# Optimization experiments

Hardware: AMD Instinct MI355X
Metric: run time of the kernel (lower is better)

Reference implementation:

```python
import jax, jax.numpy as jnp
import numpy as np

B, C, H, W = 16, 256, 128, 128  # ration = 1 -> C' = C


def setup_inputs() -> dict:
    key = jax.random.key(0)
    ks = jax.random.split(key, 7)
    s = 1.0 / np.sqrt(C)
    return {
        "x": jax.random.normal(ks[0], (B, C, H, W), dtype=jnp.float32),
        "Wq": jax.random.normal(ks[1], (C, C), dtype=jnp.float32) * s,
        "Wk": jax.random.normal(ks[2], (C, C), dtype=jnp.float32) * s,
        "Wv": jax.random.normal(ks[3], (C, C), dtype=jnp.float32) * s,
        "gamma": jax.random.normal(ks[4], (1,), dtype=jnp.float32) * 0.1,
        "Wup": jax.random.normal(ks[5], (C, C), dtype=jnp.float32) * s,
        "b_up": jax.random.normal(ks[6], (C,), dtype=jnp.float32) * 0.01,
    }


def reference(x, Wq, Wk, Wv, gamma, Wup, b_up):
    b, c, h, w = x.shape
    # 1x1 conv (no bias) == channel-mixing einsum, followed by ReLU
    proj = lambda Wm: jax.nn.relu(jnp.einsum('oc,bchw->bohw', Wm, x))
    # torch .view(B, H, -1) is a raw row-major reinterpretation of [B,C,H,W]
    q = proj(Wq).reshape(b, h, -1)                      # [B, H, C*W]
    k = proj(Wk).reshape(b, h, -1).transpose(0, 2, 1)   # [B, C*W, H]
    v = proj(Wv).reshape(b, h, -1).transpose(0, 2, 1)   # [B, C*W, H]
    # non-standard softmax over dim=1 (rows of the HxH score matrix)
    attn = jax.nn.softmax(jnp.matmul(q, k), axis=1)     # [B, H, H]
    out1 = jnp.matmul(v, attn)                          # [B, C*W, H]
    out_h = out1.reshape(b, c, h, w) * gamma            # raw reshape, gamma scale
    # layer_up: 1x1 conv with bias
    out_h = jnp.einsum('oc,bchw->bohw', Wup, out_h) + b_up[None, :, None, None]
    return (out_h, q, k, v, gamma, attn)
```

## Files before the change

kernel.cpp:

```cpp
#include <hip/hip_runtime.h>
#include <stdint.h>


typedef _Float16 f16;
typedef __attribute__((ext_vector_type(8))) _Float16 f16x8;
typedef __attribute__((ext_vector_type(4))) float f32x4;

#define DEV static __device__ __forceinline__

constexpr int  HW   = 16384;
constexpr long PB   = 4194304;
constexpr long HALF = 2097152;

constexpr long WH_OFF  = 0;
constexpr long WL_OFF  = 393216;
constexpr long WU_OFF  = 786432;
constexpr long H16_OFF = 1048576;
constexpr long WS_NEED = H16_OFF + 134217728L;

DEV unsigned pk2(float a, float b) {
  auto h = __builtin_amdgcn_cvt_pkrtz(a, b);
  return __builtin_bit_cast(unsigned, h);
}
DEV void split_pk2(float a, float b, unsigned& hu, unsigned& lu) {
  auto h = __builtin_amdgcn_cvt_pkrtz(a, b);
  auto l = __builtin_amdgcn_cvt_pkrtz(a - (float)h[0], b - (float)h[1]);
  hu = __builtin_bit_cast(unsigned, h);
  lu = __builtin_bit_cast(unsigned, l);
}
DEV f32x4 mfma16(f16x8 a, f16x8 b, f32x4 c) {
  return __builtin_amdgcn_mfma_f32_16x16x32_f16(a, b, c, 0, 0, 0);
}
DEV f16x8 ld64(const char* base, int row, int g) {
  return *(const f16x8*)(base + row * 64 + 16 * (g ^ ((row >> 1) & 3)));
}
DEV int swz64off(int row, int g) { return row * 64 + 16 * (g ^ ((row >> 1) & 3)); }

DEV void gload16(const void* g, void* l) {
  __builtin_amdgcn_global_load_lds(
      (const __attribute__((address_space(1))) uint32_t*)(g),
      (__attribute__((address_space(3))) uint32_t*)(l), 16, 0, 0);
}

DEV int swz(int row, int kbyte) {
  return (kbyte & ~63) | ((kbyte & 63) ^ (((row >> 3) & 3) << 4));
}
DEV f16x8 ldfrag(const f16* arr, int strideB, int row, int kbyte) {
  return *(const f16x8*)((const char*)arr + row * strideB + swz(row, kbyte));
}

__global__ __launch_bounds__(256) void prep_w(
    const float* __restrict__ Wq, const float* __restrict__ Wk,
    const float* __restrict__ Wv, const float* __restrict__ Wu,
    const float* __restrict__ gin, char* __restrict__ ws) {
  const int kc = blockIdx.x, m = blockIdx.y, o = threadIdx.x;
  const float* src = (m == 0) ? Wq : (m == 1) ? Wk : (m == 2) ? Wv : Wu;
  const float sc = (m == 3) ? gin[0] : 1.0f;
  float v[32];
#pragma unroll
  for (int j = 0; j < 32; ++j) v[j] = src[o * 256 + kc * 32 + j] * sc;
  char* dh = (m < 3) ? (ws + WH_OFF + ((long)(m * 8 + kc) * 256 + o) * 64)
                     : (ws + WU_OFF + ((long)kc * 256 + o) * 64);
  char* dl = ws + WL_OFF + ((long)(m * 8 + kc) * 256 + o) * 64;
  const int sw = (o >> 1) & 3;
#pragma unroll
  for (int gq = 0; gq < 4; ++gq) {
    unsigned h[4], l[4];
#pragma unroll
    for (int p = 0; p < 4; ++p)
      split_pk2(v[8 * gq + 2 * p], v[8 * gq + 2 * p + 1], h[p], l[p]);
    const int off = 16 * (gq ^ sw);
    *(uint4*)(dh + off) = make_uint4(h[0], h[1], h[2], h[3]);
    if (m < 3) *(uint4*)(dl + off) = make_uint4(l[0], l[1], l[2], l[3]);
  }
}

__global__ __launch_bounds__(256, 2) void qkv_fused2(
    const float* __restrict__ x,
    const char* __restrict__ wqh, const char* __restrict__ wql,
    const char* __restrict__ wkh, const char* __restrict__ wkl,
    const char* __restrict__ wvh,
    float* __restrict__ qseg, float* __restrict__ kseg,
    float* __restrict__ vseg) {
  __shared__ char Xh[32768];
  __shared__ char Xl[32768];
  const int t = threadIdx.x, lane = t & 63, w = t >> 6;
  const int l15 = lane & 15, g = lane >> 4;
  const int b = blockIdx.y, hw0 = blockIdx.x * 64;
  const float* xb = x + (long)b * PB + hw0;

  {
    const int hw = t & 63, cq = t >> 6;
    const int sw = (hw >> 1) & 3;
#pragma unroll
    for (int j8 = 0; j8 < 8; ++j8) {
      const int c0 = cq * 64 + j8 * 8;
      float v[8];
#pragma unroll
      for (int i = 0; i < 8; ++i) v[i] = xb[(long)(c0 + i) * HW + hw];
      unsigned h[4], l[4];
#pragma unroll
      for (int p = 0; p < 4; ++p)
        split_pk2(v[2 * p], v[2 * p + 1], h[p], l[p]);
      const int kc = c0 >> 5, gi = (c0 >> 3) & 3;
      const int off = kc * 4096 + hw * 64 + 16 * (gi ^ sw);
      *(uint4*)(Xh + off) = make_uint4(h[0], h[1], h[2], h[3]);
      *(uint4*)(Xl + off) = make_uint4(l[0], l[1], l[2], l[3]);
    }
  }
  __syncthreads();

  {
    f32x4 acc[4][4] = {};
    for (int kc = 0; kc < 8; ++kc) {
      const char* XH = Xh + kc * 4096;
      const char* XL = Xl + kc * 4096;
      const char* WH = wqh + (long)kc * 16384;
      const char* WL = wql + (long)kc * 16384;
      f16x8 bh[4], bl[4];
#pragma unroll
      for (int nf = 0; nf < 4; ++nf) {
        bh[nf] = ld64(XH, 16 * nf + l15, g);
        bl[nf] = ld64(XL, 16 * nf + l15, g);
      }
#pragma unroll
      for (int mf = 0; mf < 4; ++mf) {
        const int orow = w * 64 + 16 * mf + l15;
        f16x8 ah = ld64(WH, orow, g);
        f16x8 al = ld64(WL, orow, g);
#pragma unroll
        for (int nf = 0; nf < 4; ++nf) {
          acc[mf][nf] = mfma16(ah, bh[nf], acc[mf][nf]);
          acc[mf][nf] = mfma16(ah, bl[nf], acc[mf][nf]);
          acc[mf][nf] = mfma16(al, bh[nf], acc[mf][nf]);
        }
      }
    }
    float* ob = qseg + (long)b * PB;
#pragma unroll
    for (int mf = 0; mf < 4; ++mf)
#pragma unroll
      for (int nf = 0; nf < 4; ++nf)
#pragma unroll
        for (int r = 0; r < 4; ++r) {
          float v = acc[mf][nf][r];
          v = v > 0.f ? v : 0.f;
          const int o = w * 64 + 16 * mf + 4 * g + r;
          const int hw = hw0 + 16 * nf + l15;
          ob[(long)o * HW + hw] = v;
        }
  }

  {
    f32x4 acc[4][4] = {};
    for (int kc = 0; kc < 8; ++kc) {
      const char* XH = Xh + kc * 4096;
      const char* XL = Xl + kc * 4096;
      const char* WH = wkh + (long)kc * 16384;
      const char* WL = wkl + (long)kc * 16384;
      f16x8 bh[4], bl[4];
#pragma unroll
      for (int nf = 0; nf < 4; ++nf) {
        const int orow = w * 64 + 16 * nf + l15;
        bh[nf] = ld64(WH, orow, g);
        bl[nf] = ld64(WL, orow, g);
      }
#pragma unroll
      for (int mf = 0; mf < 4; ++mf) {
        f16x8 ah = ld64(XH, 16 * mf + l15, g);
        f16x8 al = ld64(XL, 16 * mf + l15, g);
#pragma unroll
        for (int nf = 0; nf < 4; ++nf) {
          acc[mf][nf] = mfma16(ah, bh[nf], acc[mf][nf]);
          acc[mf][nf] = mfma16(ah, bl[nf], acc[mf][nf]);
          acc[mf][nf] = mfma16(al, bh[nf], acc[mf][nf]);
        }
      }
    }
    float* ob = kseg + (long)b * PB;
#pragma unroll
    for (int mf = 0; mf < 4; ++mf)
#pragma unroll
      for (int nf = 0; nf < 4; ++nf)
#pragma unroll
        for (int r = 0; r < 4; ++r) {
          float v = acc[mf][nf][r];
          v = v > 0.f ? v : 0.f;
          const int hw = hw0 + 16 * mf + 4 * g + r;
          const int o = w * 64 + 16 * nf + l15;
          ob[((o & 1) ? HALF : 0) + (long)hw * 128 + (o >> 1)] = v;
        }
  }

  {
    f32x4 acc[4][4] = {};
    for (int kc = 0; kc < 8; ++kc) {
      const char* XH = Xh + kc * 4096;
      const char* WH = wvh + (long)kc * 16384;
      f16x8 bh[4];
#pragma unroll
      for (int nf = 0; nf < 4; ++nf)
        bh[nf] = ld64(WH, w * 64 + 16 * nf + l15, g);
#pragma unroll
      for (int mf = 0; mf < 4; ++mf) {
        f16x8 ah = ld64(XH, 16 * mf + l15, g);
#pragma unroll
        for (int nf = 0; nf < 4; ++nf)
          acc[mf][nf] = mfma16(ah, bh[nf], acc[mf][nf]);
      }
    }
    float* ob = vseg + (long)b * PB;
#pragma unroll
    for (int mf = 0; mf < 4; ++mf)
#pragma unroll
      for (int nf = 0; nf < 4; ++nf)
#pragma unroll
        for (int r = 0; r < 4; ++r) {
          float v = acc[mf][nf][r];
          v = v > 0.f ? v : 0.f;
          const int hw = hw0 + 16 * mf + 4 * g + r;
          const int o = w * 64 + 16 * nf + l15;
          ob[((o & 1) ? HALF : 0) + (long)hw * 128 + (o >> 1)] = v;
        }
  }
}

__global__ __launch_bounds__(256) void spart_kernel(
    const float* __restrict__ qseg, const float* __restrict__ kseg,
    float* __restrict__ part) {
  constexpr int SB = 80;
  __shared__ f16 Ah[128 * 40], Al[128 * 40], Bh[128 * 40], Bl[128 * 40];
  const int t = threadIdx.x, lane = t & 63, w = t >> 6;
  const int l15 = lane & 15, g = lane >> 4;
  const int ch = blockIdx.x, b = blockIdx.y;
  const float* qb = qseg + (long)b * PB + ch * 1024;
  const float* kb = kseg + (long)b * PB + (long)ch * 1024 * 128;

  f32x4 acc[4][4] = {};

  for (int kc = 0; kc < 1024; kc += 32) {
#pragma unroll
    for (int it = 0; it < 4; ++it) {
      int f4 = t + 256 * it;
      int i = f4 >> 3, c4 = f4 & 7;
      float4 v = *(const float4*)(qb + (long)i * 32768 + kc + 4 * c4);
      unsigned h01, l01, h23, l23;
      split_pk2(v.x, v.y, h01, l01);
      split_pk2(v.z, v.w, h23, l23);
      int kbo = swz(i, 8 * c4);
      *(uint2*)((char*)Ah + i * SB + kbo) = make_uint2(h01, h23);
      *(uint2*)((char*)Al + i * SB + kbo) = make_uint2(l01, l23);
    }
    {
      int c = t & 127, rh = t >> 7;
      float vs[16];
#pragma unroll
      for (int r = 0; r < 16; ++r)
        vs[r] = kb[(long)(kc + 16 * rh + r) * 128 + c];
#pragma unroll
      for (int u = 0; u < 4; ++u) {
        unsigned h0, l0, h1, l1;
        split_pk2(vs[4 * u], vs[4 * u + 1], h0, l0);
        split_pk2(vs[4 * u + 2], vs[4 * u + 3], h1, l1);
        int kbo = swz(c, 32 * rh + 8 * u);
        *(uint2*)((char*)Bh + c * SB + kbo) = make_uint2(h0, h1);
        *(uint2*)((char*)Bl + c * SB + kbo) = make_uint2(l0, l1);
      }
    }
    __syncthreads();

    f16x8 afh[4], afl[4], bfh[4], bfl[4];
#pragma unroll
    for (int f = 0; f < 4; ++f) {
      int ar = (w & 1) * 64 + 16 * f + l15;
      int br = (w >> 1) * 64 + 16 * f + l15;
      afh[f] = ldfrag(Ah, SB, ar, 16 * g);
      afl[f] = ldfrag(Al, SB, ar, 16 * g);
      bfh[f] = ldfrag(Bh, SB, br, 16 * g);
      bfl[f] = ldfrag(Bl, SB, br, 16 * g);
    }
#pragma unroll
    for (int mf = 0; mf < 4; ++mf)
#pragma unroll
      for (int nf = 0; nf < 4; ++nf) {
        acc[mf][nf] = mfma16(afh[mf], bfh[nf], acc[mf][nf]);
        acc[mf][nf] = mfma16(afh[mf], bfl[nf], acc[mf][nf]);
        acc[mf][nf] = mfma16(afl[mf], bfh[nf], acc[mf][nf]);
      }
    __syncthreads();
  }

  float* pp = part + (long)(b * 32 + ch) * 16384;
#pragma unroll
  for (int mf = 0; mf < 4; ++mf)
#pragma unroll
    for (int nf = 0; nf < 4; ++nf)
#pragma unroll
      for (int r = 0; r < 4; ++r) {
        int i = (w & 1) * 64 + 16 * mf + 4 * g + r;
        int i2 = (w >> 1) * 64 + 16 * nf + l15;
        pp[i * 128 + i2] = acc[mf][nf][r];
      }
}

__global__ __launch_bounds__(128) void reduce_s(
    const float* __restrict__ part, float* __restrict__ att,
    float* __restrict__ gout, const float* __restrict__ gin) {
  const int i = blockIdx.x, b = blockIdx.y, t = threadIdx.x;
  if (b == 0 && i == 0 && t == 0) gout[0] = gin[0];
  const float* pp = part + (long)b * 524288 + i * 128 + t;
  float s = 0.f;
#pragma unroll
  for (int c = 0; c < 32; ++c) s += pp[(long)c * 16384];
  att[((long)b * 128 + i) * 128 + t] = s;
}

__global__ __launch_bounds__(256) void softmax2(float* __restrict__ att) {
  __shared__ float red[16][17];
  const int b = blockIdx.y, c0 = blockIdx.x * 16;
  const int t = threadIdx.x, col = t & 15, ig = t >> 4;
  float* ab = att + (long)b * 16384 + c0 + col;
  float s[8];
  float m = -3.0e38f;
#pragma unroll
  for (int j = 0; j < 8; ++j) {
    s[j] = ab[(ig * 8 + j) * 128];
    m = fmaxf(m, s[j]);
  }
  red[ig][col] = m;
  __syncthreads();
  float mx = red[0][col];
#pragma unroll
  for (int k = 1; k < 16; ++k) mx = fmaxf(mx, red[k][col]);
  float sum = 0.f;
#pragma unroll
  for (int j = 0; j < 8; ++j) {
    s[j] = expf(s[j] - mx);
    sum += s[j];
  }
  __syncthreads();
  red[ig][col] = sum;
  __syncthreads();
  float tot = 0.f;
#pragma unroll
  for (int k = 0; k < 16; ++k) tot += red[k][col];
  float inv = 1.f / tot;
#pragma unroll
  for (int j = 0; j < 8; ++j) ab[(ig * 8 + j) * 128] = s[j] * inv;
}

template <int F16OUT>
__global__ __launch_bounds__(256) void out1_kernel(
    const float* __restrict__ vseg, const float* __restrict__ att,
    void* __restrict__ outp) {
  constexpr int SB = 272;
  __shared__ f16 Va[64 * 136], Ba[128 * 136];
  const int t = threadIdx.x, lane = t & 63, w = t >> 6;
  const int l15 = lane & 15, g = lane >> 4;
  const int b = blockIdx.y;
  const long j0 = (long)blockIdx.x * 64;
  const float* vb = vseg + (long)b * PB + j0 * 128;
  const float* ab = att + (long)b * 16384;

#pragma unroll
  for (int it = 0; it < 8; ++it) {
    int f4 = t + 256 * it;
    int j = f4 >> 5, c4 = f4 & 31;
    float4 v = *(const float4*)(vb + (long)j * 128 + 4 * c4);
    int kb = swz(j, 8 * c4);
    *(uint2*)((char*)Va + j * SB + kb) = make_uint2(pk2(v.x, v.y), pk2(v.z, v.w));
  }
  {
    int c = t & 127, rh = t >> 7;
#pragma unroll
    for (int uu = 0; uu < 16; ++uu) {
      int i0 = 64 * rh + 4 * uu;
      float v0 = ab[(i0 + 0) * 128 + c];
      float v1 = ab[(i0 + 1) * 128 + c];
      float v2 = ab[(i0 + 2) * 128 + c];
      float v3 = ab[(i0 + 3) * 128 + c];
      int kb = swz(c, 2 * i0);
      *(uint2*)((char*)Ba + c * SB + kb) = make_uint2(pk2(v0, v1), pk2(v2, v3));
    }
  }
  __syncthreads();

  f32x4 acc[2][4] = {};
#pragma unroll
  for (int kf = 0; kf < 4; ++kf) {
    f16x8 af[2], bf[4];
#pragma unroll
    for (int mf = 0; mf < 2; ++mf)
      af[mf] = ldfrag(Va, SB, (w & 1) * 32 + 16 * mf + l15, 64 * kf + 16 * g);
#pragma unroll
    for (int nf = 0; nf < 4; ++nf)
      bf[nf] = ldfrag(Ba, SB, (w >> 1) * 64 + 16 * nf + l15, 64 * kf + 16 * g);
#pragma unroll
    for (int mf = 0; mf < 2; ++mf)
#pragma unroll
      for (int nf = 0; nf < 4; ++nf)
        acc[mf][nf] = mfma16(af[mf], bf[nf], acc[mf][nf]);
  }

#pragma unroll
  for (int mf = 0; mf < 2; ++mf)
#pragma unroll
    for (int nf = 0; nf < 4; ++nf)
#pragma unroll
      for (int r = 0; r < 4; ++r) {
        long j = j0 + (w & 1) * 32 + 16 * mf + 4 * g + r;
        int i2 = (w >> 1) * 64 + 16 * nf + l15;
        if constexpr (F16OUT) {
          f16* ob = (f16*)outp + (long)b * PB;
          ob[j * 128 + i2] = (f16)acc[mf][nf][r];
        } else {
          float* ob = (float*)outp + (long)b * PB;
          ob[j * 128 + i2] = acc[mf][nf][r];
        }
      }
}

__global__ __launch_bounds__(256) void final3(
    float* __restrict__ outseg, const f16* __restrict__ h16,
    const char* __restrict__ wu, const float* __restrict__ bup) {
  __shared__ char lds[16384 + 4096];
  const int t = threadIdx.x, lane = t & 63, w = t >> 6;
  const int l15 = lane & 15, g = lane >> 4;
  const int b = blockIdx.y, hw0 = blockIdx.x * 64;
  const unsigned short* Hb = (const unsigned short*)(h16 + (long)b * PB);
  float* Ob = outseg + (long)b * PB;
  char* ldsA = lds;
  char* ldsB = lds + 16384;
  const int n = t & 63, rq = t >> 6;

  f32x4 acc[4][4] = {};
  for (int kc = 0; kc < 8; ++kc) {
#pragma unroll
    for (int i = 0; i < 4; ++i)
      gload16(wu + (long)kc * 16384 + w * 4096 + i * 1024 + lane * 16,
              ldsA + w * 4096 + i * 1024);
    {
      unsigned short us[8];
#pragma unroll
      for (int j = 0; j < 8; ++j)
        us[j] = Hb[(long)(kc * 32 + rq * 8 + j) * HW + hw0 + n];
      unsigned u[4];
#pragma unroll
      for (int p = 0; p < 4; ++p)
        u[p] = (unsigned)us[2 * p] | ((unsigned)us[2 * p + 1] << 16);
      *(uint4*)(ldsB + swz64off(n, rq)) = make_uint4(u[0], u[1], u[2], u[3]);
    }
    __syncthreads();
    f16x8 bf[4];
#pragma unroll
    for (int nf = 0; nf < 4; ++nf) bf[nf] = ld64(ldsB, 16 * nf + l15, g);
#pragma unroll
    for (int mf = 0; mf < 4; ++mf) {
      f16x8 af = ld64(ldsA, 64 * w + 16 * mf + l15, g);
#pragma unroll
      for (int nf = 0; nf < 4; ++nf)
        acc[mf][nf] = mfma16(af, bf[nf], acc[mf][nf]);
    }
    __syncthreads();
  }

#pragma unroll
  for (int mf = 0; mf < 4; ++mf)
#pragma unroll
    for (int nf = 0; nf < 4; ++nf)
#pragma unroll
      for (int r = 0; r < 4; ++r) {
        int o = 64 * w + 16 * mf + 4 * g + r;
        int hw = hw0 + 16 * nf + l15;
        Ob[(long)o * HW + hw] = acc[mf][nf][r] + bup[o];
      }
}

__global__ __launch_bounds__(128) void softmax_kernel(
    const float* __restrict__ part, float* __restrict__ att,
    float* __restrict__ gout, const float* __restrict__ gin) {
  const int b = blockIdx.x, t = threadIdx.x;
  if (b == 0 && t == 0) gout[0] = gin[0];
  const float* pp = part + (long)b * 32 * 16384;
  float* ab = att + (long)b * 16384;
  float mx = -3.0e38f;
  for (int i = 0; i < 128; ++i) {
    float s = 0.f;
#pragma unroll
    for (int c = 0; c < 32; ++c) s += pp[(long)c * 16384 + i * 128 + t];
    ab[i * 128 + t] = s;
    mx = fmaxf(mx, s);
  }
  float sum = 0.f;
  for (int i = 0; i < 128; ++i) {
    float e = expf(ab[i * 128 + t] - mx);
    sum += e;
    ab[i * 128 + t] = e;
  }
  float inv = 1.f / sum;
  for (int i = 0; i < 128; ++i) ab[i * 128 + t] *= inv;
}

template <int MODE>
__global__ __launch_bounds__(256) void proj_kernel(
    const float* __restrict__ x, const float* __restrict__ Wm,
    float* __restrict__ out) {
  constexpr int SB = 80;
  __shared__ f16 Wh[256 * 40];
  __shared__ f16 Wl[256 * 40];
  __shared__ f16 Xh[64 * 40];
  __shared__ f16 Xl[64 * 40];

  const int t = threadIdx.x;
  const int lane = t & 63;
  const int w = t >> 6;
  const int l15 = lane & 15;
  const int g = lane >> 4;
  const int b = blockIdx.y;
  const int hw0 = blockIdx.x * 64;
  const float* xb = x + (long)b * PB;

  f32x4 acc[4][4] = {};

  for (int kc = 0; kc < 256; kc += 32) {
#pragma unroll
    for (int it = 0; it < 8; ++it) {
      int f4 = t + 256 * it;
      int o = f4 >> 3, c4 = f4 & 7;
      float4 v = *(const float4*)(Wm + o * 256 + kc + 4 * c4);
      unsigned h01, l01, h23, l23;
      split_pk2(v.x, v.y, h01, l01);
      split_pk2(v.z, v.w, h23, l23);
      int kb = swz(o, 8 * c4);
      *(uint2*)((char*)Wh + o * SB + kb) = make_uint2(h01, h23);
      *(uint2*)((char*)Wl + o * SB + kb) = make_uint2(l01, l23);
    }
    {
      int c = t & 63, rq = t >> 6;
      float vs[8];
#pragma unroll
      for (int r = 0; r < 8; ++r)
        vs[r] = xb[(long)(kc + 8 * rq + r) * HW + hw0 + c];
#pragma unroll
      for (int u = 0; u < 2; ++u) {
        unsigned h0, l0, h1, l1;
        split_pk2(vs[4 * u], vs[4 * u + 1], h0, l0);
        split_pk2(vs[4 * u + 2], vs[4 * u + 3], h1, l1);
        int kb = swz(c, 16 * rq + 8 * u);
        *(uint2*)((char*)Xh + c * SB + kb) = make_uint2(h0, h1);
        *(uint2*)((char*)Xl + c * SB + kb) = make_uint2(l0, l1);
      }
    }
    __syncthreads();

    f16x8 wfh[4], wfl[4], xfh[4], xfl[4];
#pragma unroll
    for (int f = 0; f < 4; ++f) {
      int wr = 64 * w + 16 * f + l15;
      int xr = 16 * f + l15;
      wfh[f] = ldfrag(Wh, SB, wr, 16 * g);
      wfl[f] = ldfrag(Wl, SB, wr, 16 * g);
      xfh[f] = ldfrag(Xh, SB, xr, 16 * g);
      xfl[f] = ldfrag(Xl, SB, xr, 16 * g);
    }
#pragma unroll
    for (int mf = 0; mf < 4; ++mf)
#pragma unroll
      for (int nf = 0; nf < 4; ++nf) {
        if constexpr (MODE == 0) {
          acc[mf][nf] = mfma16(wfh[mf], xfh[nf], acc[mf][nf]);
          acc[mf][nf] = mfma16(wfh[mf], xfl[nf], acc[mf][nf]);
          acc[mf][nf] = mfma16(wfl[mf], xfh[nf], acc[mf][nf]);
        } else {
          acc[mf][nf] = mfma16(xfh[mf], wfh[nf], acc[mf][nf]);
          acc[mf][nf] = mfma16(xfh[mf], wfl[nf], acc[mf][nf]);
          acc[mf][nf] = mfma16(xfl[mf], wfh[nf], acc[mf][nf]);
        }
      }
    __syncthreads();
  }

  float* ob = out + (long)b * PB;
#pragma unroll
  for (int mf = 0; mf < 4; ++mf)
#pragma unroll
    for (int nf = 0; nf < 4; ++nf)
#pragma unroll
      for (int r = 0; r < 4; ++r) {
        float v = acc[mf][nf][r];
        v = v > 0.f ? v : 0.f;
        if constexpr (MODE == 0) {
          int o = 64 * w + 16 * mf + 4 * g + r;
          int hw = hw0 + 16 * nf + l15;
          ob[(long)o * HW + hw] = v;
        } else {
          int hw = hw0 + 16 * mf + 4 * g + r;
          int o = 64 * w + 16 * nf + l15;
          ob[((o & 1) ? HALF : 0) + (long)hw * 128 + (o >> 1)] = v;
        }
      }
}

__global__ __launch_bounds__(256) void final_kernel(
    float* __restrict__ outseg, const float* __restrict__ Wup,
    const float* __restrict__ bup, const float* __restrict__ gin) {
  constexpr int SB = 144;
  __shared__ f16 Ah[256 * 72], Bh[64 * 72];
  const int t = threadIdx.x, lane = t & 63, w = t >> 6;
  const int l15 = lane & 15, g = lane >> 4;
  const int b = blockIdx.y;
  const int hw0 = blockIdx.x * 64;
  const float gamma = gin[0];
  float* Hb = outseg + (long)b * PB;

  f32x4 acc[4][4] = {};

  for (int kc = 0; kc < 256; kc += 64) {
#pragma unroll
    for (int it = 0; it < 16; ++it) {
      int f4 = t + 256 * it;
      int o = f4 >> 4, c4 = f4 & 15;
      float4 v = *(const float4*)(Wup + o * 256 + kc + 4 * c4);
      int kb = swz(o, 8 * c4);
      *(uint2*)((char*)Ah + o * SB + kb) =
          make_uint2(pk2(v.x * gamma, v.y * gamma), pk2(v.z * gamma, v.w * gamma));
    }
    {
      int n = t & 63, rq = t >> 6;
#pragma unroll
      for (int uu = 0; uu < 4; ++uu) {
        int r0 = 16 * rq + 4 * uu;
        float v0 = Hb[(long)(kc + r0 + 0) * HW + hw0 + n];
        float v1 = Hb[(long)(kc + r0 + 1) * HW + hw0 + n];
        float v2 = Hb[(long)(kc + r0 + 2) * HW + hw0 + n];
        float v3 = Hb[(long)(kc + r0 + 3) * HW + hw0 + n];
        int kb = swz(n, 2 * r0);
        *(uint2*)((char*)Bh + n * SB + kb) = make_uint2(pk2(v0, v1), pk2(v2, v3));
      }
    }
    __syncthreads();

    f16x8 af[4][2], bf[4][2];
#pragma unroll
    for (int f = 0; f < 4; ++f)
#pragma unroll
      for (int kf = 0; kf < 2; ++kf) {
        af[f][kf] = ldfrag(Ah, SB, 64 * w + 16 * f + l15, 64 * kf + 16 * g);
        bf[f][kf] = ldfrag(Bh, SB, 16 * f + l15, 64 * kf + 16 * g);
      }
#pragma unroll
    for (int mf = 0; mf < 4; ++mf)
#pragma unroll
      for (int nf = 0; nf < 4; ++nf) {
        acc[mf][nf] = mfma16(af[mf][0], bf[nf][0], acc[mf][nf]);
        acc[mf][nf] = mfma16(af[mf][1], bf[nf][1], acc[mf][nf]);
      }
    __syncthreads();
  }

#pragma unroll
  for (int mf = 0; mf < 4; ++mf)
#pragma unroll
    for (int nf = 0; nf < 4; ++nf)
#pragma unroll
      for (int r = 0; r < 4; ++r) {
        int o = 64 * w + 16 * mf + 4 * g + r;
        int hw = hw0 + 16 * nf + l15;
        Hb[(long)o * HW + hw] = acc[mf][nf][r] + bup[o];
      }
}

extern "C" void kernel_launch(void* const* d_in, const int* in_sizes, int n_in,
                              void* d_out, int out_size, void* d_ws, size_t ws_size,
                              hipStream_t stream) {
  (void)in_sizes; (void)n_in; (void)out_size;

  const float* x  = (const float*)d_in[0];
  const float* Wq = (const float*)d_in[1];
  const float* Wk = (const float*)d_in[2];
  const float* Wv = (const float*)d_in[3];
  const float* gm = (const float*)d_in[4];
  const float* Wu = (const float*)d_in[5];
  const float* bu = (const float*)d_in[6];

  float* out  = (float*)d_out;
  float* oseg = out;
  float* qseg = out + 67108864L;
  float* kseg = out + 134217728L;
  float* vseg = out + 201326592L;
  float* gseg = out + 268435456L;
  float* aseg = out + 268435457L;

  dim3 blk(256);
  if (ws_size >= (size_t)WS_NEED && d_ws != nullptr) {
    char* ws = (char*)d_ws;
    prep_w<<<dim3(8, 4), blk, 0, stream>>>(Wq, Wk, Wv, Wu, gm, ws);
    qkv_fused2<<<dim3(256, 16), blk, 0, stream>>>(
        x, ws + WH_OFF, ws + WL_OFF, ws + WH_OFF + 131072, ws + WL_OFF + 131072,
        ws + WH_OFF + 262144, qseg, kseg, vseg);
    spart_kernel<<<dim3(32, 16), blk, 0, stream>>>(qseg, kseg, oseg);
    reduce_s<<<dim3(128, 16), dim3(128), 0, stream>>>(oseg, aseg, gseg, gm);
    softmax2<<<dim3(8, 16), blk, 0, stream>>>(aseg);
    out1_kernel<1><<<dim3(512, 16), blk, 0, stream>>>(vseg, aseg, ws + H16_OFF);
    final3<<<dim3(256, 16), blk, 0, stream>>>(
        oseg, (const f16*)(ws + H16_OFF), ws + WU_OFF, bu);
  } else {
    proj_kernel<0><<<dim3(256, 16), blk, 0, stream>>>(x, Wq, qseg);
    proj_kernel<1><<<dim3(256, 16), blk, 0, stream>>>(x, Wk, kseg);
    proj_kernel<1><<<dim3(256, 16), blk, 0, stream>>>(x, Wv, vseg);
    spart_kernel<<<dim3(32, 16), blk, 0, stream>>>(qseg, kseg, oseg);
    softmax_kernel<<<dim3(16), dim3(128), 0, stream>>>(oseg, aseg, gseg, gm);
    out1_kernel<0><<<dim3(512, 16), blk, 0, stream>>>(vseg, aseg, oseg);
    final_kernel<<<dim3(256, 16), blk, 0, stream>>>(oseg, Wu, bu, gm);
  }
}
```

Measured before the change: 707.9 us.

## Fuse attention-V matmul with up-projection and coalesce K/V stores via LDS

Replaces the separate out1 (fp16 intermediate in workspace) and final up-projection kernels with one kernel per (batch, h) row. It computes V·attn for 64-channel chunks into LDS and immediately multiplies by the fp16 Wup, so the 128 MB fp16 intermediate never goes to global memory. Separately, the K and V projection epilogues now stage ReLU results through swizzled LDS and write coalesced float4 rows instead of scattered scalar stores. The costs are extra barriers, lower occupancy from large LDS use, and a serial chunk loop inside the fused kernel.

Result: faster. 672.6 us (-5.0%).

```diff
diff --git a/kernel.cpp b/kernel.cpp
--- a/kernel.cpp
+++ b/kernel.cpp
@@ -15,8 +15,7 @@
 constexpr long WH_OFF  = 0;
 constexpr long WL_OFF  = 393216;
 constexpr long WU_OFF  = 786432;
-constexpr long H16_OFF = 1048576;
-constexpr long WS_NEED = H16_OFF + 134217728L;
+constexpr long WS_NEED = 1048576;
 
 DEV unsigned pk2(float a, float b) {
   auto h = __builtin_amdgcn_cvt_pkrtz(a, b);
@@ -34,7 +33,6 @@
 DEV f16x8 ld64(const char* base, int row, int g) {
   return *(const f16x8*)(base + row * 64 + 16 * (g ^ ((row >> 1) & 3)));
 }
-DEV int swz64off(int row, int g) { return row * 64 + 16 * (g ^ ((row >> 1) & 3)); }
 
 DEV void gload16(const void* g, void* l) {
   __builtin_amdgcn_global_load_lds(
@@ -75,15 +73,17 @@
   }
 }
 
-__global__ __launch_bounds__(256, 2) void qkv_fused2(
+__global__ __launch_bounds__(256, 2) void qkv_fused3(
     const float* __restrict__ x,
     const char* __restrict__ wqh, const char* __restrict__ wql,
     const char* __restrict__ wkh, const char* __restrict__ wkl,
     const char* __restrict__ wvh,
     float* __restrict__ qseg, float* __restrict__ kseg,
     float* __restrict__ vseg) {
-  __shared__ char Xh[32768];
-  __shared__ char Xl[32768];
+  __shared__ char lds[65536];
+  char* Xh = lds;
+  char* Xl = lds + 32768;
+  float* R = (float*)(lds + 32768);
   const int t = threadIdx.x, lane = t & 63, w = t >> 6;
   const int l15 = lane & 15, g = lane >> 4;
   const int b = blockIdx.y, hw0 = blockIdx.x * 64;
@@ -109,6 +109,37 @@
     }
   }
   __syncthreads();
+
+  auto repack_store = [&](f32x4 (&ac)[4][4], float* ob) {
+#pragma unroll
+    for (int half = 0; half < 2; ++half) {
+#pragma unroll
+      for (int mf2 = 0; mf2 < 2; ++mf2) {
+        const int mf = 2 * half + mf2;
+#pragma unroll
+        for (int nf = 0; nf < 4; ++nf)
+#pragma unroll
+          for (int r = 0; r < 4; ++r) {
+            const int hwloc = 16 * mf2 + 4 * g + r;
+            const int o = w * 64 + 16 * nf + l15;
+            const int col = (o >> 1) ^ (((hwloc >> 2) & 3) << 3);
+            float v = ac[mf][nf][r];
+            R[(o & 1) * 4096 + hwloc * 128 + col] = v > 0.f ? v : 0.f;
+          }
+      }
+      __syncthreads();
+#pragma unroll
+      for (int it = 0; it < 8; ++it) {
+        const int f = t + 256 * it;
+        const int parity = f >> 10, hwloc = (f >> 5) & 31, q4 = f & 31;
+        const int col = (4 * q4) ^ (((hwloc >> 2) & 3) << 3);
+        const float4 v4 = *(const float4*)(R + parity * 4096 + hwloc * 128 + col);
+        *(float4*)(ob + (long)parity * HALF +
+                   (long)(hw0 + 32 * half + hwloc) * 128 + 4 * q4) = v4;
+      }
+      __syncthreads();
+    }
+  };
 
   {
     f32x4 acc[4][4] = {};
@@ -177,19 +208,8 @@
         }
       }
     }
-    float* ob = kseg + (long)b * PB;
-#pragma unroll
-    for (int mf = 0; mf < 4; ++mf)
-#pragma unroll
-      for (int nf = 0; nf < 4; ++nf)
-#pragma unroll
-        for (int r = 0; r < 4; ++r) {
-          float v = acc[mf][nf][r];
-          v = v > 0.f ? v : 0.f;
-          const int hw = hw0 + 16 * mf + 4 * g + r;
-          const int o = w * 64 + 16 * nf + l15;
-          ob[((o & 1) ? HALF : 0) + (long)hw * 128 + (o >> 1)] = v;
-        }
+    __syncthreads();
+    repack_store(acc, kseg + (long)b * PB);
   }
 
   {
@@ -209,19 +229,7 @@
           acc[mf][nf] = mfma16(ah, bh[nf], acc[mf][nf]);
       }
     }
-    float* ob = vseg + (long)b * PB;
-#pragma unroll
-    for (int mf = 0; mf < 4; ++mf)
-#pragma unroll
-      for (int nf = 0; nf < 4; ++nf)
-#pragma unroll
-        for (int r = 0; r < 4; ++r) {
-          float v = acc[mf][nf][r];
-          v = v > 0.f ? v : 0.f;
-          const int hw = hw0 + 16 * mf + 4 * g + r;
-          const int o = w * 64 + 16 * nf + l15;
-          ob[((o & 1) ? HALF : 0) + (long)hw * 128 + (o >> 1)] = v;
-        }
+    repack_store(acc, vseg + (long)b * PB);
   }
 }
 
@@ -349,130 +357,98 @@
   for (int j = 0; j < 8; ++j) ab[(ig * 8 + j) * 128] = s[j] * inv;
 }
 
-template <int F16OUT>
-__global__ __launch_bounds__(256) void out1_kernel(
+__global__ __launch_bounds__(256, 2) void pvf_fused(
     const float* __restrict__ vseg, const float* __restrict__ att,
-    void* __restrict__ outp) {
-  constexpr int SB = 272;
-  __shared__ f16 Va[64 * 136], Ba[128 * 136];
+    const char* __restrict__ wu, const float* __restrict__ bup,
+    float* __restrict__ oseg) {
+  __shared__ char attnT[128 * 272];
+  __shared__ char vA[64 * 272];
+  __shared__ char HT[128 * 144];
   const int t = threadIdx.x, lane = t & 63, w = t >> 6;
   const int l15 = lane & 15, g = lane >> 4;
-  const int b = blockIdx.y;
-  const long j0 = (long)blockIdx.x * 64;
-  const float* vb = vseg + (long)b * PB + j0 * 128;
+  const int b = blockIdx.y, h = blockIdx.x;
   const float* ab = att + (long)b * 16384;
-
-#pragma unroll
-  for (int it = 0; it < 8; ++it) {
-    int f4 = t + 256 * it;
-    int j = f4 >> 5, c4 = f4 & 31;
-    float4 v = *(const float4*)(vb + (long)j * 128 + 4 * c4);
-    int kb = swz(j, 8 * c4);
-    *(uint2*)((char*)Va + j * SB + kb) = make_uint2(pk2(v.x, v.y), pk2(v.z, v.w));
-  }
-  {
-    int c = t & 127, rh = t >> 7;
-#pragma unroll
-    for (int uu = 0; uu < 16; ++uu) {
-      int i0 = 64 * rh + 4 * uu;
-      float v0 = ab[(i0 + 0) * 128 + c];
-      float v1 = ab[(i0 + 1) * 128 + c];
-      float v2 = ab[(i0 + 2) * 128 + c];
-      float v3 = ab[(i0 + 3) * 128 + c];
-      int kb = swz(c, 2 * i0);
-      *(uint2*)((char*)Ba + c * SB + kb) = make_uint2(pk2(v0, v1), pk2(v2, v3));
-    }
-  }
-  __syncthreads();
-
-  f32x4 acc[2][4] = {};
-#pragma unroll
-  for (int kf = 0; kf < 4; ++kf) {
-    f16x8 af[2], bf[4];
-#pragma unroll
-    for (int mf = 0; mf < 2; ++mf)
-      af[mf] = ldfrag(Va, SB, (w & 1) * 32 + 16 * mf + l15, 64 * kf + 16 * g);
-#pragma unroll
-    for (int nf = 0; nf < 4; ++nf)
-      bf[nf] = ldfrag(Ba, SB, (w >> 1) * 64 + 16 * nf + l15, 64 * kf + 16 * g);
-#pragma unroll
-    for (int mf = 0; mf < 2; ++mf)
-#pragma unroll
-      for (int nf = 0; nf < 4; ++nf)
-        acc[mf][nf] = mfma16(af[mf], bf[nf], acc[mf][nf]);
-  }
-
-#pragma unroll
-  for (int mf = 0; mf < 2; ++mf)
-#pragma unroll
-    for (int nf = 0; nf < 4; ++nf)
+  const float* vb = vseg + (long)b * PB;
+  float* Ob = oseg + (long)b * PB;
+
+#pragma unroll
+  for (int it = 0; it < 4; ++it) {
+    const int f = t + 256 * it;
+    const int i4 = f >> 5, w4 = f & 31;
+    const float4 r0 = *(const float4*)(ab + (4 * i4 + 0) * 128 + 4 * w4);
+    const float4 r1 = *(const float4*)(ab + (4 * i4 + 1) * 128 + 4 * w4);
+    const float4 r2 = *(const float4*)(ab + (4 * i4 + 2) * 128 + 4 * w4);
+    const float4 r3 = *(const float4*)(ab + (4 * i4 + 3) * 128 + 4 * w4);
+    *(uint2*)(attnT + (4 * w4 + 0) * 272 + swz(4 * w4 + 0, 8 * i4)) =
+        make_uint2(pk2(r0.x, r1.x), pk2(r2.x, r3.x));
+    *(uint2*)(attnT + (4 * w4 + 1) * 272 + swz(4 * w4 + 1, 8 * i4)) =
+        make_uint2(pk2(r0.y, r1.y), pk2(r2.y, r3.y));
+    *(uint2*)(attnT + (4 * w4 + 2) * 272 + swz(4 * w4 + 2, 8 * i4)) =
+        make_uint2(pk2(r0.z, r1.z), pk2(r2.z, r3.z));
+    *(uint2*)(attnT + (4 * w4 + 3) * 272 + swz(4 * w4 + 3, 8 * i4)) =
+        make_uint2(pk2(r0.w, r1.w), pk2(r2.w, r3.w));
+  }
+
+  f32x4 acc2[4][8] = {};
+
+  for (int cc = 0; cc < 4; ++cc) {
+#pragma unroll
+    for (int it = 0; it < 8; ++it) {
+      const int f = t + 256 * it;
+      const int cp = f >> 5, q4 = f & 31;
+      const float4 v4 =
+          *(const float4*)(vb + ((long)(cc * 64 + cp) * 128 + h) * 128 + 4 * q4);
+      *(uint2*)(vA + cp * 272 + swz(cp, 8 * q4)) =
+          make_uint2(pk2(v4.x, v4.y), pk2(v4.z, v4.w));
+    }
+    __syncthreads();
+
+    f32x4 acc1[8] = {};
+#pragma unroll
+    for (int kf = 0; kf < 4; ++kf) {
+      const f16x8 a = ldfrag((const f16*)vA, 272, w * 16 + l15, 64 * kf + 16 * g);
+#pragma unroll
+      for (int nf = 0; nf < 8; ++nf) {
+        const f16x8 bf = ldfrag((const f16*)attnT, 272, 16 * nf + l15, 64 * kf + 16 * g);
+        acc1[nf] = mfma16(a, bf, acc1[nf]);
+      }
+    }
+#pragma unroll
+    for (int nf = 0; nf < 8; ++nf)
 #pragma unroll
       for (int r = 0; r < 4; ++r) {
-        long j = j0 + (w & 1) * 32 + 16 * mf + 4 * g + r;
-        int i2 = (w >> 1) * 64 + 16 * nf + l15;
-        if constexpr (F16OUT) {
-          f16* ob = (f16*)outp + (long)b * PB;
-          ob[j * 128 + i2] = (f16)acc[mf][nf][r];
-        } else {
-          float* ob = (float*)outp + (long)b * PB;
-          ob[j * 128 + i2] = acc[mf][nf][r];
-        }
-      }
-}
-
-__global__ __launch_bounds__(256) void final3(
-    float* __restrict__ outseg, const f16* __restrict__ h16,
-    const char* __restrict__ wu, const float* __restrict__ bup) {
-  __shared__ char lds[16384 + 4096];
-  const int t = threadIdx.x, lane = t & 63, w = t >> 6;
-  const int l15 = lane & 15, g = lane >> 4;
-  const int b = blockIdx.y, hw0 = blockIdx.x * 64;
-  const unsigned short* Hb = (const unsigned short*)(h16 + (long)b * PB);
-  float* Ob = outseg + (long)b * PB;
-  char* ldsA = lds;
-  char* ldsB = lds + 16384;
-  const int n = t & 63, rq = t >> 6;
-
-  f32x4 acc[4][4] = {};
-  for (int kc = 0; kc < 8; ++kc) {
-#pragma unroll
-    for (int i = 0; i < 4; ++i)
-      gload16(wu + (long)kc * 16384 + w * 4096 + i * 1024 + lane * 16,
-              ldsA + w * 4096 + i * 1024);
-    {
-      unsigned short us[8];
-#pragma unroll
-      for (int j = 0; j < 8; ++j)
-        us[j] = Hb[(long)(kc * 32 + rq * 8 + j) * HW + hw0 + n];
-      unsigned u[4];
-#pragma unroll
-      for (int p = 0; p < 4; ++p)
-        u[p] = (unsigned)us[2 * p] | ((unsigned)us[2 * p + 1] << 16);
-      *(uint4*)(ldsB + swz64off(n, rq)) = make_uint4(u[0], u[1], u[2], u[3]);
-    }
-    __syncthreads();
-    f16x8 bf[4];
-#pragma unroll
-    for (int nf = 0; nf < 4; ++nf) bf[nf] = ld64(ldsB, 16 * nf + l15, g);
-#pragma unroll
-    for (int mf = 0; mf < 4; ++mf) {
-      f16x8 af = ld64(ldsA, 64 * w + 16 * mf + l15, g);
-#pragma unroll
-      for (int nf = 0; nf < 4; ++nf)
-        acc[mf][nf] = mfma16(af, bf[nf], acc[mf][nf]);
-    }
-    __syncthreads();
+        const int wp = 16 * nf + l15;
+        const int cp = w * 16 + 4 * g + r;
+        *(f16*)(HT + wp * 144 + swz(wp, 2 * cp)) = (f16)acc1[nf][r];
+      }
+    __syncthreads();
+
+#pragma unroll
+    for (int kf2 = 0; kf2 < 2; ++kf2) {
+      const char* WU = wu + (long)(cc * 2 + kf2) * 16384;
+      f16x8 af[4];
+#pragma unroll
+      for (int mf = 0; mf < 4; ++mf)
+        af[mf] = ld64(WU, w * 64 + 16 * mf + l15, g);
+#pragma unroll
+      for (int nf = 0; nf < 8; ++nf) {
+        const f16x8 bf = ldfrag((const f16*)HT, 144, 16 * nf + l15, 64 * kf2 + 16 * g);
+#pragma unroll
+        for (int mf = 0; mf < 4; ++mf)
+          acc2[mf][nf] = mfma16(af[mf], bf, acc2[mf][nf]);
+      }
+    }
   }
 
 #pragma unroll
   for (int mf = 0; mf < 4; ++mf)
 #pragma unroll
-    for (int nf = 0; nf < 4; ++nf)
+    for (int nf = 0; nf < 8; ++nf)
 #pragma unroll
       for (int r = 0; r < 4; ++r) {
-        int o = 64 * w + 16 * mf + 4 * g + r;
-        int hw = hw0 + 16 * nf + l15;
-        Ob[(long)o * HW + hw] = acc[mf][nf][r] + bup[o];
+        const int o = w * 64 + 16 * mf + 4 * g + r;
+        const int wp = 16 * nf + l15;
+        Ob[(long)o * HW + h * 128 + wp] = acc2[mf][nf][r] + bup[o];
       }
 }
 
@@ -601,6 +577,71 @@
       }
 }
 
+__global__ __launch_bounds__(256) void out1_fb(
+    const float* __restrict__ vseg, const float* __restrict__ att,
+    float* __restrict__ outseg) {
+  constexpr int SB = 272;
+  __shared__ f16 Va[64 * 136], Ba[128 * 136];
+  const int t = threadIdx.x, lane = t & 63, w = t >> 6;
+  const int l15 = lane & 15, g = lane >> 4;
+  const int b = blockIdx.y;
+  const long j0 = (long)blockIdx.x * 64;
+  const float* vb = vseg + (long)b * PB + j0 * 128;
+  const float* ab = att + (long)b * 16384;
+
+#pragma unroll
+  for (int it = 0; it < 8; ++it) {
+    int f4 = t + 256 * it;
+    int j = f4 >> 5, c4 = f4 & 31;
+    float4 v = *(const float4*)(vb + (long)j * 128 + 4 * c4);
+    int kb = swz(j, 8 * c4);
+    *(uint2*)((char*)Va + j * SB + kb) = make_uint2(pk2(v.x, v.y), pk2(v.z, v.w));
+  }
+  {
+    int c = t & 127, rh = t >> 7;
+#pragma unroll
+    for (int uu = 0; uu < 16; ++uu) {
+      int i0 = 64 * rh + 4 * uu;
+      float v0 = ab[(i0 + 0) * 128 + c];
+      float v1 = ab[(i0 + 1) * 128 + c];
+      float v2 = ab[(i0 + 2) * 128 + c];
+      float v3 = ab[(i0 + 3) * 128 + c];
+      int kb = swz(c, 2 * i0);
+      *(uint2*)((char*)Ba + c * SB + kb) = make_uint2(pk2(v0, v1), pk2(v2, v3));
+    }
+  }
+  __syncthreads();
+
+  f32x4 acc[2][4] = {};
+#pragma unroll
+  for (int kf = 0; kf < 4; ++kf) {
+    f16x8 af[2], bf[4];
+#pragma unroll
+    for (int mf = 0; mf < 2; ++mf)
+      af[mf] = ldfrag(Va, SB, (w & 1) * 32 + 16 * mf + l15, 64 * kf + 16 * g);
+#pragma unroll
+    for (int nf = 0; nf < 4; ++nf)
+      bf[nf] = ldfrag(Ba, SB, (w >> 1) * 64 + 16 * nf + l15, 64 * kf + 16 * g);
+#pragma unroll
+    for (int mf = 0; mf < 2; ++mf)
+#pragma unroll
+      for (int nf = 0; nf < 4; ++nf)
+        acc[mf][nf] = mfma16(af[mf], bf[nf], acc[mf][nf]);
+  }
+
+  float* ob = outseg + (long)b * PB;
+#pragma unroll
+  for (int mf = 0; mf < 2; ++mf)
+#pragma unroll
+    for (int nf = 0; nf < 4; ++nf)
+#pragma unroll
+      for (int r = 0; r < 4; ++r) {
+        long j = j0 + (w & 1) * 32 + 16 * mf + 4 * g + r;
+        int i2 = (w >> 1) * 64 + 16 * nf + l15;
+        ob[j * 128 + i2] = acc[mf][nf][r];
+      }
+}
+
 __global__ __launch_bounds__(256) void final_kernel(
     float* __restrict__ outseg, const float* __restrict__ Wup,
     const float* __restrict__ bup, const float* __restrict__ gin) {
@@ -695,22 +736,20 @@
   if (ws_size >= (size_t)WS_NEED && d_ws != nullptr) {
     char* ws = (char*)d_ws;
     prep_w<<<dim3(8, 4), blk, 0, stream>>>(Wq, Wk, Wv, Wu, gm, ws);
-    qkv_fused2<<<dim3(256, 16), blk, 0, stream>>>(
+    qkv_fused3<<<dim3(256, 16), blk, 0, stream>>>(
         x, ws + WH_OFF, ws + WL_OFF, ws + WH_OFF + 131072, ws + WL_OFF + 131072,
         ws + WH_OFF + 262144, qseg, kseg, vseg);
     spart_kernel<<<dim3(32, 16), blk, 0, stream>>>(qseg, kseg, oseg);
     reduce_s<<<dim3(128, 16), dim3(128), 0, stream>>>(oseg, aseg, gseg, gm);
     softmax2<<<dim3(8, 16), blk, 0, stream>>>(aseg);
-    out1_kernel<1><<<dim3(512, 16), blk, 0, stream>>>(vseg, aseg, ws + H16_OFF);
-    final3<<<dim3(256, 16), blk, 0, stream>>>(
-        oseg, (const f16*)(ws + H16_OFF), ws + WU_OFF, bu);
+    pvf_fused<<<dim3(128, 16), blk, 0, stream>>>(vseg, aseg, ws + WU_OFF, bu, oseg);
   } else {
     proj_kernel<0><<<dim3(256, 16), blk, 0, stream>>>(x, Wq, qseg);
     proj_kernel<1><<<dim3(256, 16), blk, 0, stream>>>(x, Wk, kseg);
     proj_kernel<1><<<dim3(256, 16), blk, 0, stream>>>(x, Wv, vseg);
     spart_kernel<<<dim3(32, 16), blk, 0, stream>>>(qseg, kseg, oseg);
     softmax_kernel<<<dim3(16), dim3(128), 0, stream>>>(oseg, aseg, gseg, gm);
-    out1_kernel<0><<<dim3(512, 16), blk, 0, stream>>>(vseg, aseg, oseg);
+    out1_fb<<<dim3(512, 16), blk, 0, stream>>>(vseg, aseg, oseg);
     final_kernel<<<dim3(256, 16), blk, 0, stream>>>(oseg, Wu, bu, gm);
   }
 }
```
